# Kernel optimization log

Hardware: AMD Instinct MI355X
Metric: run time of the kernel (lower is better)

Reference implementation:

```python
import jax, jax.numpy as jnp
import numpy as np

QP = 127.0          # 2**(8-1)-1, signed symmetric int8
MIN_RANGE = 1e-6


def _ste_round(x):
    # round_pass: forward round, straight-through gradient
    return x + jax.lax.stop_gradient(jnp.round(x) - x)


def _quant_per_tensor(x):
    # symmetric per-tensor: scale = max|x| / Qp (grad flows through max as in source)
    scale = jnp.maximum(jnp.max(jnp.abs(x)), MIN_RANGE) / QP
    return _ste_round(x / scale), scale


def _qlinear(x2d, w, b):
    # faithful to _quantize_global (prefix_token_num=None path):
    #   out = (x_q @ w_q.T + bias) * (s_w * s_x)
    xq, sx = _quant_per_tensor(x2d)
    wq, sw = _quant_per_tensor(w)
    out = jnp.matmul(xq, wq.T) + b[None, :]
    return out * (sw * sx)


def setup_inputs() -> dict:
    key = jax.random.key(0)
    k = jax.random.split(key, 5)
    B, N, D, H = 8, 1024, 1024, 4096
    return {
        "x": jax.random.normal(k[0], (B, N, D), dtype=jnp.float32),
        "w1": jax.random.normal(k[1], (H, D), dtype=jnp.float32) * 0.02,
        "b1": jax.random.normal(k[2], (H,), dtype=jnp.float32) * 0.02,
        "w2": jax.random.normal(k[3], (D, H), dtype=jnp.float32) * 0.02,
        "b2": jax.random.normal(k[4], (D,), dtype=jnp.float32) * 0.02,
    }


def reference(x, w1, b1, w2, b2):
    B, N, D = x.shape
    h = _qlinear(x.reshape(-1, D), w1, b1)          # [B*N, H]
    h = jax.nn.gelu(h, approximate=False)            # exact GELU (nn.GELU default)
    o = _qlinear(h, w2, b2)                          # [B*N, D]
    return o.reshape(B, N, -1)
```

## Files before the change

kernel.cpp:

```cpp
#include <hip/hip_runtime.h>
#include <cstdint>
#include <cmath>

#define QP    127.0f
#define MINR  1e-6f

#define MTOK 8192
#define DDIM 1024
#define HDIM 4096

typedef __attribute__((ext_vector_type(4))) int int32x4;

__device__ __forceinline__ void gload16(const void* g, void* l) {
    __builtin_amdgcn_global_load_lds(
        (const __attribute__((address_space(1))) void*)g,
        (__attribute__((address_space(3))) void*)l, 16, 0, 0);
}

__global__ void zero_scales_kernel(float* g) {
    if (threadIdx.x < 4) g[threadIdx.x] = 0.0f;
}

__device__ __forceinline__ float wave_block_max(float m) {
    #pragma unroll
    for (int off = 32; off; off >>= 1) m = fmaxf(m, __shfl_down(m, off));
    __shared__ float sm[4];
    int lane = threadIdx.x & 63, w = threadIdx.x >> 6;
    if (lane == 0) sm[w] = m;
    __syncthreads();
    float bm = 0.0f;
    if (threadIdx.x == 0) bm = fmaxf(fmaxf(sm[0], sm[1]), fmaxf(sm[2], sm[3]));
    return bm;
}

__device__ __forceinline__ void absmax_range(const float4* in4, int n4, int bid, int nb,
                                             float* gout) {
    int tid = bid * blockDim.x + threadIdx.x;
    int stride = nb * blockDim.x;
    float m = 0.0f;
    for (int i = tid; i < n4; i += stride) {
        float4 v = in4[i];
        m = fmaxf(m, fmaxf(fmaxf(fabsf(v.x), fabsf(v.y)), fmaxf(fabsf(v.z), fabsf(v.w))));
    }
    float bm = wave_block_max(m);
    if (threadIdx.x == 0) atomicMax((int*)gout, __float_as_int(bm));
}

__global__ void absmax3_kernel(const float* __restrict__ x, const float* __restrict__ w1,
                               const float* __restrict__ w2, float* __restrict__ gmax) {
    int b = blockIdx.x;
    if (b < 1024)      absmax_range((const float4*)x,  MTOK * DDIM / 4, b,        1024, gmax + 0);
    else if (b < 1536) absmax_range((const float4*)w1, HDIM * DDIM / 4, b - 1024,  512, gmax + 1);
    else               absmax_range((const float4*)w2, DDIM * HDIM / 4, b - 1536,  512, gmax + 3);
}

__device__ __forceinline__ void quant_range(const float4* in4, int* out4, int n4,
                                            int bid, int nb, const float* gm) {
    const float s = fmaxf(*gm, MINR) / QP;
    int tid = bid * blockDim.x + threadIdx.x;
    int stride = nb * blockDim.x;
    for (int i = tid; i < n4; i += stride) {
        float4 v = in4[i];
        int q0 = ((int)rintf(v.x / s)) & 255;
        int q1 = ((int)rintf(v.y / s)) & 255;
        int q2 = ((int)rintf(v.z / s)) & 255;
        int q3 = ((int)rintf(v.w / s)) & 255;
        out4[i] = q0 | (q1 << 8) | (q2 << 16) | (q3 << 24);
    }
}

__global__ void quant3_kernel(const float* __restrict__ x, const float* __restrict__ w1,
                              const float* __restrict__ w2, int8_t* __restrict__ xq,
                              int8_t* __restrict__ w1q, int8_t* __restrict__ w2q,
                              const float* __restrict__ gmax) {
    int b = blockIdx.x;
    if (b < 2048)      quant_range((const float4*)x,  (int*)xq,  MTOK * DDIM / 4, b,        2048, gmax + 0);
    else if (b < 3072) quant_range((const float4*)w1, (int*)w1q, HDIM * DDIM / 4, b - 2048, 1024, gmax + 1);
    else               quant_range((const float4*)w2, (int*)w2q, DDIM * HDIM / 4, b - 3072, 1024, gmax + 3);
}

__global__ void quant_kernel(const float* __restrict__ in, int8_t* __restrict__ out,
                             int n4, const float* __restrict__ gm) {
    quant_range((const float4*)in, (int*)out, n4, blockIdx.x, gridDim.x, gm);
}

template<int KD, int ND, bool GELU_EPI>
__global__ __launch_bounds__(256, 3)
void gemm_i8_kernel(const int8_t* __restrict__ A, const int8_t* __restrict__ B,
                    const float* __restrict__ bias,
                    const float* __restrict__ gmA, const float* __restrict__ gmB,
                    float* __restrict__ out, float* __restrict__ omax) {
    __shared__ int8_t lA[128 * 128];
    __shared__ int8_t lB[128 * 128];
    const int t = threadIdx.x;
    const int lane = t & 63;
    const int w = t >> 6;
    const int wm = (w >> 1) * 64;
    const int wn = (w & 1) * 64;
    const int lr = lane & 15;
    const int lg = lane >> 4;

    const int chunk = gridDim.x >> 3;
    const int logical = (blockIdx.x & 7) * chunk + (blockIdx.x >> 3);
    const int br = logical & 63;
    const int bc = logical >> 6;

    const int8_t* Ab = A + (size_t)br * 128 * KD;
    const int8_t* Bb = B + (size_t)bc * 128 * KD;

    int32x4 acc[4][4] = {};

    for (int kt = 0; kt < KD / 128; ++kt) {
        #pragma unroll
        for (int i = 0; i < 4; ++i) {
            int c = t + i * 256;
            int r = c >> 3;
            int sl = c & 7;
            int sc = ((sl ^ (r & 7)) << 4);
            gload16(Ab + (size_t)r * KD + kt * 128 + sc, &lA[c * 16]);
            gload16(Bb + (size_t)r * KD + kt * 128 + sc, &lB[c * 16]);
        }
        __syncthreads();

        #pragma unroll
        for (int kk = 0; kk < 2; ++kk) {
            int32x4 af[4], bf[4];
            #pragma unroll
            for (int m = 0; m < 4; ++m) {
                int r = wm + m * 16 + lr;
                int g = kk * 4 + lg;
                af[m] = *(const int32x4*)&lA[r * 128 + ((g ^ (r & 7)) << 4)];
            }
            #pragma unroll
            for (int n = 0; n < 4; ++n) {
                int r = wn + n * 16 + lr;
                int g = kk * 4 + lg;
                bf[n] = *(const int32x4*)&lB[r * 128 + ((g ^ (r & 7)) << 4)];
            }
            #pragma unroll
            for (int m = 0; m < 4; ++m)
                #pragma unroll
                for (int n = 0; n < 4; ++n)
                    acc[m][n] = __builtin_amdgcn_mfma_i32_16x16x64_i8(af[m], bf[n], acc[m][n], 0, 0, 0);
        }
        __syncthreads();
    }

    const float sA = fmaxf(*gmA, MINR) / QP;
    const float sB = fmaxf(*gmB, MINR) / QP;
    const float s = sB * sA;
    float lmax = 0.0f;
    #pragma unroll
    for (int m = 0; m < 4; ++m) {
        #pragma unroll
        for (int n = 0; n < 4; ++n) {
            #pragma unroll
            for (int r = 0; r < 4; ++r) {
                int row = br * 128 + wm + m * 16 + lg * 4 + r;
                int col = bc * 128 + wn + n * 16 + lr;
                float f = (float)acc[m][n][r] + bias[col];
                f *= s;
                if (GELU_EPI) {
                    float gg = f * (erff(f / 1.41421356237309504880f) + 1.0f) * 0.5f;
                    out[(size_t)row * ND + col] = gg;
                    lmax = fmaxf(lmax, fabsf(gg));
                } else {
                    out[(size_t)row * ND + col] = f;
                }
            }
        }
    }
    if (GELU_EPI) {
        #pragma unroll
        for (int off = 32; off; off >>= 1) lmax = fmaxf(lmax, __shfl_down(lmax, off));
        __shared__ float red[4];
        if (lane == 0) red[w] = lmax;
        __syncthreads();
        if (t == 0) {
            float bm = fmaxf(fmaxf(red[0], red[1]), fmaxf(red[2], red[3]));
            atomicMax((int*)omax, __float_as_int(bm));
        }
    }
}

extern "C" void kernel_launch(void* const* d_in, const int* in_sizes, int n_in,
                              void* d_out, int out_size, void* d_ws, size_t ws_size,
                              hipStream_t stream) {
    const float* x  = (const float*)d_in[0];
    const float* w1 = (const float*)d_in[1];
    const float* b1 = (const float*)d_in[2];
    const float* w2 = (const float*)d_in[3];
    const float* b2 = (const float*)d_in[4];
    float* out = (float*)d_out;

    uint8_t* ws = (uint8_t*)d_ws;
    float*  gmax = (float*)ws;
    int8_t* xq   = (int8_t*)(ws + 256);
    int8_t* w1q  = xq  + (size_t)MTOK * DDIM;
    int8_t* w2q  = w1q + (size_t)HDIM * DDIM;
    int8_t* hq   = w2q + (size_t)DDIM * HDIM;
    float*  h    = (float*)(hq + (size_t)MTOK * HDIM);

    zero_scales_kernel<<<1, 64, 0, stream>>>(gmax);

    absmax3_kernel<<<2048, 256, 0, stream>>>(x, w1, w2, gmax);
    quant3_kernel<<<4096, 256, 0, stream>>>(x, w1, w2, xq, w1q, w2q, gmax);

    gemm_i8_kernel<DDIM, HDIM, true>
        <<<2048, 256, 0, stream>>>(xq, w1q, b1, gmax + 0, gmax + 1, h, gmax + 2);

    quant_kernel<<<4096, 256, 0, stream>>>(h, hq, MTOK * HDIM / 4, gmax + 2);

    gemm_i8_kernel<HDIM, DDIM, false>
        <<<512, 256, 0, stream>>>(hq, w2q, b2, gmax + 2, gmax + 3, out, nullptr);
}
```

Measured before the change: 208.3 us.

## Pre-pack int8 operands into MFMA fragment layout and drop LDS staging in GEMM

The quantize kernels now write int8 data in a tiled 16x64 fragment-major layout that matches the MFMA operand pattern. This lets the GEMM load fragments straight from global memory into registers, with no LDS staging and no barriers. The goal is to remove LDS traffic and synchronisation overhead. The cost is that each wave now reads operands directly from global/L2 with no reuse across waves, which raises cache and memory pressure and exposes load latency without explicit pipelining. The block-to-tile mapping also changes from row-major to column-first ordering.

```diff
diff --git a/kernel.cpp b/kernel.cpp
--- a/kernel.cpp
+++ b/kernel.cpp
@@ -10,12 +10,6 @@
 #define HDIM 4096
 
 typedef __attribute__((ext_vector_type(4))) int int32x4;
-
-__device__ __forceinline__ void gload16(const void* g, void* l) {
-    __builtin_amdgcn_global_load_lds(
-        (const __attribute__((address_space(1))) void*)g,
-        (__attribute__((address_space(3))) void*)l, 16, 0, 0);
-}
 
 __global__ void zero_scales_kernel(float* g) {
     if (threadIdx.x < 4) g[threadIdx.x] = 0.0f;
@@ -54,18 +48,33 @@
     else               absmax_range((const float4*)w2, DDIM * HDIM / 4, b - 1536,  512, gmax + 3);
 }
 
-__device__ __forceinline__ void quant_range(const float4* in4, int* out4, int n4,
-                                            int bid, int nb, const float* gm) {
+__device__ __forceinline__ int pack4(float4 v, float s) {
+    return (((int)rintf(v.x / s)) & 255) | ((((int)rintf(v.y / s)) & 255) << 8) |
+           ((((int)rintf(v.z / s)) & 255) << 16) | ((((int)rintf(v.w / s)) & 255) << 24);
+}
+
+template<int K>
+__device__ __forceinline__ void quant_pack_range(const float* __restrict__ in,
+                                                 int8_t* __restrict__ out, int R,
+                                                 int bid, int nb,
+                                                 const float* __restrict__ gm) {
     const float s = fmaxf(*gm, MINR) / QP;
+    const float4* in4 = (const float4*)in;
+    const int total = (R / 16) * (K / 16) * 16;
     int tid = bid * blockDim.x + threadIdx.x;
     int stride = nb * blockDim.x;
-    for (int i = tid; i < n4; i += stride) {
-        float4 v = in4[i];
-        int q0 = ((int)rintf(v.x / s)) & 255;
-        int q1 = ((int)rintf(v.y / s)) & 255;
-        int q2 = ((int)rintf(v.z / s)) & 255;
-        int q3 = ((int)rintf(v.w / s)) & 255;
-        out4[i] = q0 | (q1 << 8) | (q2 << 16) | (q3 << 24);
+    for (int i = tid; i < total; i += stride) {
+        int ib = i << 4;
+        int r = ib / K;
+        int k0 = ib & (K - 1);
+        int32x4 q;
+        q[0] = pack4(in4[i * 4 + 0], s);
+        q[1] = pack4(in4[i * 4 + 1], s);
+        q[2] = pack4(in4[i * 4 + 2], s);
+        q[3] = pack4(in4[i * 4 + 3], s);
+        size_t off = ((size_t)((r >> 4) * (K >> 6) + (k0 >> 6)) << 10)
+                   + ((r & 15) << 6) + (k0 & 63);
+        *(int32x4*)(out + off) = q;
     }
 }
 
@@ -74,24 +83,24 @@
                               int8_t* __restrict__ w1q, int8_t* __restrict__ w2q,
                               const float* __restrict__ gmax) {
     int b = blockIdx.x;
-    if (b < 2048)      quant_range((const float4*)x,  (int*)xq,  MTOK * DDIM / 4, b,        2048, gmax + 0);
-    else if (b < 3072) quant_range((const float4*)w1, (int*)w1q, HDIM * DDIM / 4, b - 2048, 1024, gmax + 1);
-    else               quant_range((const float4*)w2, (int*)w2q, DDIM * HDIM / 4, b - 3072, 1024, gmax + 3);
-}
-
-__global__ void quant_kernel(const float* __restrict__ in, int8_t* __restrict__ out,
-                             int n4, const float* __restrict__ gm) {
-    quant_range((const float4*)in, (int*)out, n4, blockIdx.x, gridDim.x, gm);
+    if (b < 2048)      quant_pack_range<DDIM>(x,  xq,  MTOK, b,        2048, gmax + 0);
+    else if (b < 3072) quant_pack_range<DDIM>(w1, w1q, HDIM, b - 2048, 1024, gmax + 1);
+    else               quant_pack_range<HDIM>(w2, w2q, DDIM, b - 3072, 1024, gmax + 3);
+}
+
+__global__ void quant_h_kernel(const float* __restrict__ h, int8_t* __restrict__ hq,
+                               const float* __restrict__ gm) {
+    quant_pack_range<HDIM>(h, hq, MTOK, blockIdx.x, gridDim.x, gm);
 }
 
 template<int KD, int ND, bool GELU_EPI>
 __global__ __launch_bounds__(256, 3)
-void gemm_i8_kernel(const int8_t* __restrict__ A, const int8_t* __restrict__ B,
+void gemm_i8_direct(const int8_t* __restrict__ A, const int8_t* __restrict__ B,
                     const float* __restrict__ bias,
                     const float* __restrict__ gmA, const float* __restrict__ gmB,
                     float* __restrict__ out, float* __restrict__ omax) {
-    __shared__ int8_t lA[128 * 128];
-    __shared__ int8_t lB[128 * 128];
+    constexpr int KP = KD >> 6;
+    constexpr int NBC = ND / 128;
     const int t = threadIdx.x;
     const int lane = t & 63;
     const int w = t >> 6;
@@ -102,48 +111,29 @@
 
     const int chunk = gridDim.x >> 3;
     const int logical = (blockIdx.x & 7) * chunk + (blockIdx.x >> 3);
-    const int br = logical & 63;
-    const int bc = logical >> 6;
-
-    const int8_t* Ab = A + (size_t)br * 128 * KD;
-    const int8_t* Bb = B + (size_t)bc * 128 * KD;
+    const int bc = logical % NBC;
+    const int br = logical / NBC;
+
+    const int lo = lr * 64 + lg * 16;
+    const int8_t* Ap = A + ((size_t)((br * 8 + (wm >> 4)) * KP) << 10) + lo;
+    const int8_t* Bp = B + ((size_t)((bc * 8 + (wn >> 4)) * KP) << 10) + lo;
 
     int32x4 acc[4][4] = {};
 
-    for (int kt = 0; kt < KD / 128; ++kt) {
-        #pragma unroll
-        for (int i = 0; i < 4; ++i) {
-            int c = t + i * 256;
-            int r = c >> 3;
-            int sl = c & 7;
-            int sc = ((sl ^ (r & 7)) << 4);
-            gload16(Ab + (size_t)r * KD + kt * 128 + sc, &lA[c * 16]);
-            gload16(Bb + (size_t)r * KD + kt * 128 + sc, &lB[c * 16]);
-        }
-        __syncthreads();
-
-        #pragma unroll
-        for (int kk = 0; kk < 2; ++kk) {
-            int32x4 af[4], bf[4];
+    #pragma unroll 2
+    for (int kp = 0; kp < KP; ++kp) {
+        int32x4 af[4], bf[4];
+        #pragma unroll
+        for (int m = 0; m < 4; ++m)
+            af[m] = *(const int32x4*)(Ap + ((size_t)(m * KP + kp) << 10));
+        #pragma unroll
+        for (int n = 0; n < 4; ++n)
+            bf[n] = *(const int32x4*)(Bp + ((size_t)(n * KP + kp) << 10));
+        #pragma unroll
+        for (int m = 0; m < 4; ++m)
             #pragma unroll
-            for (int m = 0; m < 4; ++m) {
-                int r = wm + m * 16 + lr;
-                int g = kk * 4 + lg;
-                af[m] = *(const int32x4*)&lA[r * 128 + ((g ^ (r & 7)) << 4)];
-            }
-            #pragma unroll
-            for (int n = 0; n < 4; ++n) {
-                int r = wn + n * 16 + lr;
-                int g = kk * 4 + lg;
-                bf[n] = *(const int32x4*)&lB[r * 128 + ((g ^ (r & 7)) << 4)];
-            }
-            #pragma unroll
-            for (int m = 0; m < 4; ++m)
-                #pragma unroll
-                for (int n = 0; n < 4; ++n)
-                    acc[m][n] = __builtin_amdgcn_mfma_i32_16x16x64_i8(af[m], bf[n], acc[m][n], 0, 0, 0);
-        }
-        __syncthreads();
+            for (int n = 0; n < 4; ++n)
+                acc[m][n] = __builtin_amdgcn_mfma_i32_16x16x64_i8(af[m], bf[n], acc[m][n], 0, 0, 0);
     }
 
     const float sA = fmaxf(*gmA, MINR) / QP;
@@ -206,11 +196,11 @@
     absmax3_kernel<<<2048, 256, 0, stream>>>(x, w1, w2, gmax);
     quant3_kernel<<<4096, 256, 0, stream>>>(x, w1, w2, xq, w1q, w2q, gmax);
 
-    gemm_i8_kernel<DDIM, HDIM, true>
+    gemm_i8_direct<DDIM, HDIM, true>
         <<<2048, 256, 0, stream>>>(xq, w1q, b1, gmax + 0, gmax + 1, h, gmax + 2);
 
-    quant_kernel<<<4096, 256, 0, stream>>>(h, hq, MTOK * HDIM / 4, gmax + 2);
-
-    gemm_i8_kernel<HDIM, DDIM, false>
+    quant_h_kernel<<<4096, 256, 0, stream>>>(h, hq, gmax + 2);
+
+    gemm_i8_direct<HDIM, DDIM, false>
         <<<512, 256, 0, stream>>>(hq, w2q, b2, gmax + 2, gmax + 3, out, nullptr);
 }
```

Result: slower. 272.1 us (+30.6%).

## Double-buffer LDS tiles in int8 GEMM and switch to a 2D grid

Applied to the files above, without the earlier changes.

Adds a two-stage LDS ping-pong to the int8 MFMA GEMM, so the next K-tile is prefetched with global_load_lds while the current tile is computed, with one barrier per iteration instead of two. LDS per block doubles to 64 KB, so launch bounds drop from 3 to 2 blocks per CU. The XCD-aware block remapping is replaced by a plain 2D grid, which changes L2 locality across XCDs. The GELU reduction scratch now reuses the A tile buffer, with an extra barrier.

```diff
diff --git a/kernel.cpp b/kernel.cpp
--- a/kernel.cpp
+++ b/kernel.cpp
@@ -15,6 +15,11 @@
     __builtin_amdgcn_global_load_lds(
         (const __attribute__((address_space(1))) void*)g,
         (__attribute__((address_space(3))) void*)l, 16, 0, 0);
+}
+
+__device__ __forceinline__ void barrier_fence() {
+    __builtin_amdgcn_s_barrier();
+    asm volatile("" ::: "memory");
 }
 
 __global__ void zero_scales_kernel(float* g) {
@@ -85,13 +90,14 @@
 }
 
 template<int KD, int ND, bool GELU_EPI>
-__global__ __launch_bounds__(256, 3)
+__global__ __launch_bounds__(256, 2)
 void gemm_i8_kernel(const int8_t* __restrict__ A, const int8_t* __restrict__ B,
                     const float* __restrict__ bias,
                     const float* __restrict__ gmA, const float* __restrict__ gmB,
                     float* __restrict__ out, float* __restrict__ omax) {
-    __shared__ int8_t lA[128 * 128];
-    __shared__ int8_t lB[128 * 128];
+    constexpr int KT = KD / 128;
+    __shared__ int8_t lA[2 * 128 * 128];
+    __shared__ int8_t lB[2 * 128 * 128];
     const int t = threadIdx.x;
     const int lane = t & 63;
     const int w = t >> 6;
@@ -99,29 +105,25 @@
     const int wn = (w & 1) * 64;
     const int lr = lane & 15;
     const int lg = lane >> 4;
-
-    const int chunk = gridDim.x >> 3;
-    const int logical = (blockIdx.x & 7) * chunk + (blockIdx.x >> 3);
-    const int br = logical & 63;
-    const int bc = logical >> 6;
+    const int br = blockIdx.y, bc = blockIdx.x;
 
     const int8_t* Ab = A + (size_t)br * 128 * KD;
     const int8_t* Bb = B + (size_t)bc * 128 * KD;
 
     int32x4 acc[4][4] = {};
 
-    for (int kt = 0; kt < KD / 128; ++kt) {
+    auto stage = [&](int s, int kt) {
         #pragma unroll
         for (int i = 0; i < 4; ++i) {
             int c = t + i * 256;
             int r = c >> 3;
             int sl = c & 7;
             int sc = ((sl ^ (r & 7)) << 4);
-            gload16(Ab + (size_t)r * KD + kt * 128 + sc, &lA[c * 16]);
-            gload16(Bb + (size_t)r * KD + kt * 128 + sc, &lB[c * 16]);
-        }
-        __syncthreads();
-
+            gload16(Ab + (size_t)r * KD + kt * 128 + sc, &lA[s * 16384 + c * 16]);
+            gload16(Bb + (size_t)r * KD + kt * 128 + sc, &lB[s * 16384 + c * 16]);
+        }
+    };
+    auto compute = [&](int s) {
         #pragma unroll
         for (int kk = 0; kk < 2; ++kk) {
             int32x4 af[4], bf[4];
@@ -129,13 +131,13 @@
             for (int m = 0; m < 4; ++m) {
                 int r = wm + m * 16 + lr;
                 int g = kk * 4 + lg;
-                af[m] = *(const int32x4*)&lA[r * 128 + ((g ^ (r & 7)) << 4)];
+                af[m] = *(const int32x4*)&lA[s * 16384 + r * 128 + ((g ^ (r & 7)) << 4)];
             }
             #pragma unroll
             for (int n = 0; n < 4; ++n) {
                 int r = wn + n * 16 + lr;
                 int g = kk * 4 + lg;
-                bf[n] = *(const int32x4*)&lB[r * 128 + ((g ^ (r & 7)) << 4)];
+                bf[n] = *(const int32x4*)&lB[s * 16384 + r * 128 + ((g ^ (r & 7)) << 4)];
             }
             #pragma unroll
             for (int m = 0; m < 4; ++m)
@@ -143,7 +145,19 @@
                 for (int n = 0; n < 4; ++n)
                     acc[m][n] = __builtin_amdgcn_mfma_i32_16x16x64_i8(af[m], bf[n], acc[m][n], 0, 0, 0);
         }
-        __syncthreads();
+    };
+
+    stage(0, 0);
+    asm volatile("s_waitcnt vmcnt(0)" ::: "memory");
+    barrier_fence();
+
+    int cur = 0;
+    for (int kt = 0; kt < KT; ++kt) {
+        if (kt + 1 < KT) stage(cur ^ 1, kt + 1);
+        compute(cur);
+        if (kt + 1 < KT) asm volatile("s_waitcnt vmcnt(0)" ::: "memory");
+        barrier_fence();
+        cur ^= 1;
     }
 
     const float sA = fmaxf(*gmA, MINR) / QP;
@@ -173,7 +187,8 @@
     if (GELU_EPI) {
         #pragma unroll
         for (int off = 32; off; off >>= 1) lmax = fmaxf(lmax, __shfl_down(lmax, off));
-        __shared__ float red[4];
+        float* red = (float*)lA;
+        __syncthreads();
         if (lane == 0) red[w] = lmax;
         __syncthreads();
         if (t == 0) {
@@ -207,10 +222,10 @@
     quant3_kernel<<<4096, 256, 0, stream>>>(x, w1, w2, xq, w1q, w2q, gmax);
 
     gemm_i8_kernel<DDIM, HDIM, true>
-        <<<2048, 256, 0, stream>>>(xq, w1q, b1, gmax + 0, gmax + 1, h, gmax + 2);
+        <<<dim3(32, 64), 256, 0, stream>>>(xq, w1q, b1, gmax + 0, gmax + 1, h, gmax + 2);
 
     quant_kernel<<<4096, 256, 0, stream>>>(h, hq, MTOK * HDIM / 4, gmax + 2);
 
     gemm_i8_kernel<HDIM, DDIM, false>
-        <<<512, 256, 0, stream>>>(hq, w2q, b2, gmax + 2, gmax + 3, out, nullptr);
-}
+        <<<dim3(8, 64), 256, 0, stream>>>(hq, w2q, b2, gmax + 2, gmax + 3, out, nullptr);
+}
```

After: 212.2 us. No clear change (+1.9%).

## Store GELU intermediate in fp16 and quantize from half precision

Applied to the files above, without the earlier changes.

The first GEMM now writes the GELU intermediate as fp16 instead of fp32, which halves the write traffic and the re-read traffic of the 8192x4096 intermediate. A new quant kernel reads eight halves per thread. The block-index mapping now puts columns inner, and launch bounds drop from 3 to 2 waves per SIMD. The risk is that fp16 rounding of h can flip int8 rounding for values near a boundary, while the absmax is still taken from the fp32 values.

```diff
diff --git a/kernel.cpp b/kernel.cpp
--- a/kernel.cpp
+++ b/kernel.cpp
@@ -1,4 +1,5 @@
 #include <hip/hip_runtime.h>
+#include <hip/hip_fp16.h>
 #include <cstdint>
 #include <cmath>
 
@@ -10,6 +11,7 @@
 #define HDIM 4096
 
 typedef __attribute__((ext_vector_type(4))) int int32x4;
+typedef __attribute__((ext_vector_type(8))) short short8;
 
 __device__ __forceinline__ void gload16(const void* g, void* l) {
     __builtin_amdgcn_global_load_lds(
@@ -79,17 +81,37 @@
     else               quant_range((const float4*)w2, (int*)w2q, DDIM * HDIM / 4, b - 3072, 1024, gmax + 3);
 }
 
-__global__ void quant_kernel(const float* __restrict__ in, int8_t* __restrict__ out,
-                             int n4, const float* __restrict__ gm) {
-    quant_range((const float4*)in, (int*)out, n4, blockIdx.x, gridDim.x, gm);
-}
-
-template<int KD, int ND, bool GELU_EPI>
-__global__ __launch_bounds__(256, 3)
+__global__ void quant_h_kernel(const __half* __restrict__ h, int8_t* __restrict__ hq,
+                               const float* __restrict__ gm) {
+    const float s = fmaxf(*gm, MINR) / QP;
+    const short8* in8 = (const short8*)h;
+    int2* out8 = (int2*)hq;
+    const int n8 = MTOK * HDIM / 8;
+    int tid = blockIdx.x * blockDim.x + threadIdx.x;
+    int stride = gridDim.x * blockDim.x;
+    for (int i = tid; i < n8; i += stride) {
+        short8 v = in8[i];
+        int q[8];
+        #pragma unroll
+        for (int j = 0; j < 8; ++j) {
+            __half_raw r; r.x = (unsigned short)v[j];
+            float f = __half2float(__half(r));
+            q[j] = ((int)rintf(f / s)) & 255;
+        }
+        int2 o;
+        o.x = q[0] | (q[1] << 8) | (q[2] << 16) | (q[3] << 24);
+        o.y = q[4] | (q[5] << 8) | (q[6] << 16) | (q[7] << 24);
+        out8[i] = o;
+    }
+}
+
+template<int KD, int ND, bool GELU_EPI, typename OUTT>
+__global__ __launch_bounds__(256, 2)
 void gemm_i8_kernel(const int8_t* __restrict__ A, const int8_t* __restrict__ B,
                     const float* __restrict__ bias,
                     const float* __restrict__ gmA, const float* __restrict__ gmB,
-                    float* __restrict__ out, float* __restrict__ omax) {
+                    OUTT* __restrict__ out, float* __restrict__ omax) {
+    constexpr int NBC = ND / 128;
     __shared__ int8_t lA[128 * 128];
     __shared__ int8_t lB[128 * 128];
     const int t = threadIdx.x;
@@ -102,8 +124,8 @@
 
     const int chunk = gridDim.x >> 3;
     const int logical = (blockIdx.x & 7) * chunk + (blockIdx.x >> 3);
-    const int br = logical & 63;
-    const int bc = logical >> 6;
+    const int bc = logical % NBC;
+    const int br = logical / NBC;
 
     const int8_t* Ab = A + (size_t)br * 128 * KD;
     const int8_t* Bb = B + (size_t)bc * 128 * KD;
@@ -162,10 +184,10 @@
                 f *= s;
                 if (GELU_EPI) {
                     float gg = f * (erff(f / 1.41421356237309504880f) + 1.0f) * 0.5f;
-                    out[(size_t)row * ND + col] = gg;
+                    out[(size_t)row * ND + col] = (OUTT)gg;
                     lmax = fmaxf(lmax, fabsf(gg));
                 } else {
-                    out[(size_t)row * ND + col] = f;
+                    out[(size_t)row * ND + col] = (OUTT)f;
                 }
             }
         }
@@ -199,18 +221,18 @@
     int8_t* w1q  = xq  + (size_t)MTOK * DDIM;
     int8_t* w2q  = w1q + (size_t)HDIM * DDIM;
     int8_t* hq   = w2q + (size_t)DDIM * HDIM;
-    float*  h    = (float*)(hq + (size_t)MTOK * HDIM);
+    __half* h    = (__half*)(hq + (size_t)MTOK * HDIM);
 
     zero_scales_kernel<<<1, 64, 0, stream>>>(gmax);
 
     absmax3_kernel<<<2048, 256, 0, stream>>>(x, w1, w2, gmax);
     quant3_kernel<<<4096, 256, 0, stream>>>(x, w1, w2, xq, w1q, w2q, gmax);
 
-    gemm_i8_kernel<DDIM, HDIM, true>
+    gemm_i8_kernel<DDIM, HDIM, true, __half>
         <<<2048, 256, 0, stream>>>(xq, w1q, b1, gmax + 0, gmax + 1, h, gmax + 2);
 
-    quant_kernel<<<4096, 256, 0, stream>>>(h, hq, MTOK * HDIM / 4, gmax + 2);
-
-    gemm_i8_kernel<HDIM, DDIM, false>
+    quant_h_kernel<<<2048, 256, 0, stream>>>(h, hq, gmax + 2);
+
+    gemm_i8_kernel<HDIM, DDIM, false, float>
         <<<512, 256, 0, stream>>>(hq, w2q, b2, gmax + 2, gmax + 3, out, nullptr);
 }
```

Result: faster. 193.0 us (-7.4%).
